# Optimization experiments

Hardware: AMD Instinct MI355X
Metric: run time of the kernel (lower is better)

Reference implementation:

```python
import jax, jax.numpy as jnp
import numpy as np

EPS = 1e-6
K = 20
NUM_OBJECTS = 50
OBJ_FEAT = 256
C_DIM = 128
HIDDEN = 128


def vn_linear(x, W):
    # x: [B, C, 3, ...]; W: [O, C] -> [B, O, 3, ...]
    return jnp.einsum('oc,bc...->bo...', W, x)


def vn_leaky(x, Wdir, slope):
    d = vn_linear(x, Wdir)
    dot = jnp.sum(x * d, axis=2, keepdims=True)
    dsq = jnp.sum(d * d, axis=2, keepdims=True)
    x_neg = x - (dot / (dsq + EPS)) * d
    return slope * x + (1.0 - slope) * jnp.where(dot >= 0, x, x_neg)


def vn_linear_leaky(x, Wfeat, Wdir, slope):
    pf = vn_linear(x, Wfeat)
    d = vn_linear(x, Wdir)
    dot = jnp.sum(pf * d, axis=2, keepdims=True)
    dsq = jnp.sum(d * d, axis=2, keepdims=True)
    p_neg = pf - (dot / (dsq + EPS)) * d
    return slope * pf + (1.0 - slope) * jnp.where(dot >= 0, pf, p_neg)


def resblock(x, fc0, fc1, a0, a1, sc):
    net = vn_linear(vn_leaky(x, a0, 0.0), fc0)
    dx = vn_linear(vn_leaky(net, a1, 0.0), fc1)
    return vn_linear(x, sc) + dx


def get_graph_feature_cross(x, k):
    # x: [B, 3, N] -> edge features [B, 3, 3, N, k]
    inner = -2.0 * jnp.einsum('bdn,bdm->bnm', x, x)
    xx = jnp.sum(x * x, axis=1)                       # [B, N]
    neg_dist = -xx[:, :, None] - inner - xx[:, None, :]  # [B, N, N]
    idx = jax.lax.top_k(neg_dist, k)[1]               # [B, N, k] nearest neighbors
    xt = jnp.transpose(x, (0, 2, 1))                  # [B, N, 3]
    nbr = jax.vmap(lambda pts, ind: pts[ind])(xt, idx)  # [B, N, k, 3]
    ctr = jnp.broadcast_to(xt[:, :, None, :], nbr.shape)
    cross = jnp.cross(nbr, ctr)
    feat = jnp.stack([nbr - ctr, ctr, cross], axis=3)  # [B, N, k, 3, 3]
    return jnp.transpose(feat, (0, 3, 4, 1, 2))


def mlp2(zf, w0, w1, w2):
    h = jax.nn.relu(zf @ w0.T)
    h = jax.nn.relu(h @ w1.T)
    return h @ w2.T


def setup_inputs():
    key = jax.random.key(0)
    ks = jax.random.split(key, 24)
    B, N = 4, 4096

    def rn(k, shape):
        return jax.random.normal(k, shape, dtype=jnp.float32) * (1.0 / np.sqrt(shape[-1]))

    return {
        'p': jax.random.normal(ks[0], (B, N, 3), dtype=jnp.float32),
        'z_idxs': jax.random.randint(ks[1], (B,), 0, NUM_OBJECTS),
        'z': jax.random.normal(ks[2], (NUM_OBJECTS, OBJ_FEAT), dtype=jnp.float32),
        'hw0': rn(ks[3], (OBJ_FEAT, OBJ_FEAT)),
        'hw1': rn(ks[4], (OBJ_FEAT, OBJ_FEAT)),
        'hw2': rn(ks[5], (C_DIM * HIDDEN, OBJ_FEAT)),
        'hb0': rn(ks[6], (OBJ_FEAT, OBJ_FEAT)),
        'hb1': rn(ks[7], (OBJ_FEAT, OBJ_FEAT)),
        'hb2': rn(ks[8], (C_DIM, OBJ_FEAT)),
        'conv_pos_feat': rn(ks[9], (128, 3)),
        'conv_pos_dir': rn(ks[10], (128, 3)),
        'fc_pos_w': rn(ks[11], (2 * HIDDEN, 128)),
        'blk_fc0': rn(ks[12], (5, HIDDEN, 2 * HIDDEN)),
        'blk_fc1': rn(ks[13], (5, HIDDEN, HIDDEN)),
        'blk_act0': rn(ks[14], (5, 2 * HIDDEN, 2 * HIDDEN)),
        'blk_act1': rn(ks[15], (5, HIDDEN, HIDDEN)),
        'blk_sc': rn(ks[16], (5, HIDDEN, 2 * HIDDEN)),
        'actc_dir': rn(ks[17], (HIDDEN, HIDDEN)),
    }


def reference(p, z_idxs, z, hw0, hw1, hw2, hb0, hb1, hb2, conv_pos_feat,
              conv_pos_dir, fc_pos_w, blk_fc0, blk_fc1, blk_act0, blk_act1,
              blk_sc, actc_dir):
    B = p.shape[0]
    x = jnp.transpose(p, (0, 2, 1))                       # [B, 3, N]
    feat = get_graph_feature_cross(x, K)                  # [B, 3, 3, N, k]
    net = vn_linear_leaky(feat, conv_pos_feat, conv_pos_dir, 0.2)  # [B,128,3,N,k]
    net = jnp.mean(net, axis=-1)                          # [B,128,3,N]
    net = vn_linear(net, fc_pos_w)                        # [B,256,3,N]
    for i in range(5):
        net = resblock(net, blk_fc0[i], blk_fc1[i], blk_act0[i], blk_act1[i], blk_sc[i])
        if i < 4:
            pooled = jnp.mean(net, axis=-1, keepdims=True)
            net = jnp.concatenate([net, jnp.broadcast_to(pooled, net.shape)], axis=1)
    net = vn_leaky(jnp.mean(net, axis=-1), actc_dir, 0.2)  # [B, HIDDEN, 3]
    zf = z[z_idxs]                                        # [B, OBJ_FEAT]
    w = mlp2(zf, hw0, hw1, hw2).reshape(B, C_DIM, HIDDEN)  # hypernet weights
    b = mlp2(zf, hb0, hb1, hb2)                           # [B, C_DIM]
    c = jnp.einsum('bhd,bch->bcd', net, w) + b[:, :, None]  # [B, C_DIM, 3]
    return c
```

## Files before the change

kernel.cpp:

```cpp
#include <hip/hip_runtime.h>
#include <hip/hip_fp16.h>
#include <cstdint>
#include <cstddef>

#define NPTS 4096
#define BATCH 4
#define KNN 20

typedef __half f16;
using f32x4 = __attribute__((ext_vector_type(4))) float;
using f16x8 = __attribute__((ext_vector_type(8))) _Float16;

__device__ inline void gload_lds16(const void* g, void* l) {
    __builtin_amdgcn_global_load_lds(
        (const __attribute__((address_space(1))) uint32_t*)g,
        (__attribute__((address_space(3))) uint32_t*)l, 16, 0, 0);
}

__global__ __launch_bounds__(256) void knn_kernel(const float* __restrict__ p,
                                                  int* __restrict__ idx_out) {
    __shared__ float smem[12288];
    float* pts = smem;
    unsigned* lists = (unsigned*)smem;
    const int tid  = threadIdx.x;
    const int wave = tid >> 6, lane = tid & 63;
    const int b  = blockIdx.x >> 10;
    const int nb = ((blockIdx.x & 1023) << 2) + wave;

    const float4* src4 = (const float4*)(p + (size_t)b * NPTS * 3);
    float4* dst4 = (float4*)pts;
    for (int i = tid; i < NPTS * 3 / 4; i += 256) dst4[i] = src4[i];
    __syncthreads();

    const float cx = pts[3 * nb], cy = pts[3 * nb + 1], cz = pts[3 * nb + 2];
    unsigned lst[4];
#pragma unroll
    for (int i = 0; i < 4; i++) lst[i] = 0xFFFFFFFFu;

    for (int t = 0; t < NPTS / 64; t++) {
        int m = (t << 6) + lane;
        float dx = pts[3 * m] - cx, dy = pts[3 * m + 1] - cy, dz = pts[3 * m + 2] - cz;
        float d = dx * dx + dy * dy + dz * dz;
        unsigned c = (__float_as_uint(d) & 0xFFFFF000u) | (unsigned)m;
#pragma unroll
        for (int j = 0; j < 4; j++) {
            unsigned lo = min(c, lst[j]);
            c = max(c, lst[j]);
            lst[j] = lo;
        }
    }
    __syncthreads();
#pragma unroll
    for (int i = 0; i < 4; i++) lists[tid * 5 + i] = lst[i];
    __syncthreads();

    int head = 0;
    const size_t out_base = ((size_t)b * NPTS + nb) * KNN;
    for (int r = 0; r < KNN; r++) {
        unsigned cand = (head < 4) ? lists[tid * 5 + head] : 0xFFFFFFFFu;
        unsigned win = cand;
#pragma unroll
        for (int off = 32; off > 0; off >>= 1) {
            unsigned o = (unsigned)__shfl_xor((int)win, off, 64);
            win = o < win ? o : win;
        }
        if (cand == win) head++;
        if (lane == 0) idx_out[out_base + r] = (int)(win & 0xFFFu);
    }
}

__global__ __launch_bounds__(128) void edgeconv_kernel(
    const float* __restrict__ p, const int* __restrict__ idx,
    const float* __restrict__ wf, const float* __restrict__ wd,
    f16* __restrict__ out) {
    __shared__ float e[KNN][9];
    const int col = blockIdx.x;
    const int b = col >> 12;
    const int tid = threadIdx.x;
    const float cx = p[(size_t)col * 3], cy = p[(size_t)col * 3 + 1], cz = p[(size_t)col * 3 + 2];
    if (tid < KNN) {
        int j = idx[(size_t)col * KNN + tid];
        const float* q = &p[((size_t)b * NPTS + j) * 3];
        float nx = q[0], ny = q[1], nz = q[2];
        e[tid][0] = nx - cx; e[tid][1] = ny - cy; e[tid][2] = nz - cz;
        e[tid][3] = cx;      e[tid][4] = cy;      e[tid][5] = cz;
        e[tid][6] = ny * cz - nz * cy;
        e[tid][7] = nz * cx - nx * cz;
        e[tid][8] = nx * cy - ny * cx;
    }
    __syncthreads();
    const int o = tid;
    const float f0 = wf[o * 3], f1 = wf[o * 3 + 1], f2 = wf[o * 3 + 2];
    const float g0 = wd[o * 3], g1 = wd[o * 3 + 1], g2 = wd[o * 3 + 2];
    float a0 = 0.f, a1 = 0.f, a2 = 0.f;
    for (int k = 0; k < KNN; k++) {
        float pf[3], dd[3];
#pragma unroll
        for (int s = 0; s < 3; s++) {
            pf[s] = f0 * e[k][s] + f1 * e[k][3 + s] + f2 * e[k][6 + s];
            dd[s] = g0 * e[k][s] + g1 * e[k][3 + s] + g2 * e[k][6 + s];
        }
        float dot = pf[0] * dd[0] + pf[1] * dd[1] + pf[2] * dd[2];
        float dsq = dd[0] * dd[0] + dd[1] * dd[1] + dd[2] * dd[2];
        float coef = dot / (dsq + 1e-6f);
        bool pos = dot >= 0.f;
        float v0 = pos ? pf[0] : pf[0] - coef * dd[0];
        float v1 = pos ? pf[1] : pf[1] - coef * dd[1];
        float v2 = pos ? pf[2] : pf[2] - coef * dd[2];
        a0 += 0.2f * pf[0] + 0.8f * v0;
        a1 += 0.2f * pf[1] + 0.8f * v1;
        a2 += 0.2f * pf[2] + 0.8f * v2;
    }
    const float inv = 1.f / (float)KNN;
    out[((size_t)col * 3 + 0) * 128 + o] = __float2half(a0 * inv);
    out[((size_t)col * 3 + 1) * 128 + o] = __float2half(a1 * inv);
    out[((size_t)col * 3 + 2) * 128 + o] = __float2half(a2 * inv);
}

__global__ __launch_bounds__(256) void gemm_mfma(
    const uint16_t* __restrict__ A, const uint16_t* __restrict__ W,
    f16* __restrict__ Y, int K, int O, int lda, int ldw) {
    __shared__ char lds[65536];
    const int tid = threadIdx.x;
    const int wid = tid >> 6, lane = tid & 63;
    const int r0 = blockIdx.x * 128, c0 = blockIdx.y * 128;
    const int wm = (wid >> 1) * 64, wn = (wid & 1) * 64;

    f32x4 acc[4][4];
#pragma unroll
    for (int i = 0; i < 4; i++)
#pragma unroll
        for (int j = 0; j < 4; j++) acc[i][j] = (f32x4){0.f, 0.f, 0.f, 0.f};

    const int srow = (lane >> 3);
    const int scol = ((lane & 7) ^ srow) * 8;

    auto STAGE = [&](int bf, int kc) {
        char* As = lds + bf * 32768;
        char* Bs = As + 16384;
#pragma unroll
        for (int t = 0; t < 4; t++) {
            int chunk = t * 4 + wid;
            int row = chunk * 8 + srow;
            gload_lds16(&A[(size_t)(r0 + row) * lda + kc + scol], As + chunk * 1024);
            gload_lds16(&W[(size_t)(c0 + row) * ldw + kc + scol], Bs + chunk * 1024);
        }
    };
    auto COMPUTE = [&](int bf) {
        char* As = lds + bf * 32768;
        char* Bs = As + 16384;
#pragma unroll
        for (int kb = 0; kb < 2; kb++) {
            const int kl = (kb * 32 + (lane >> 4) * 8) * 2;
            f16x8 af[4], bfr[4];
#pragma unroll
            for (int mi = 0; mi < 4; mi++) {
                int r = wm + mi * 16 + (lane & 15);
                af[mi] = *(const f16x8*)(As + r * 128 + (kl ^ ((r & 7) << 4)));
            }
#pragma unroll
            for (int ni = 0; ni < 4; ni++) {
                int r = wn + ni * 16 + (lane & 15);
                bfr[ni] = *(const f16x8*)(Bs + r * 128 + (kl ^ ((r & 7) << 4)));
            }
#pragma unroll
            for (int mi = 0; mi < 4; mi++)
#pragma unroll
                for (int ni = 0; ni < 4; ni++)
                    acc[mi][ni] = __builtin_amdgcn_mfma_f32_16x16x32_f16(
                        af[mi], bfr[ni], acc[mi][ni], 0, 0, 0);
        }
    };

    STAGE(0, 0);
    __syncthreads();
    int cur = 0;
    const int nt = K >> 6;
    for (int t = 0; t < nt; t++) {
        if (t + 1 < nt) STAGE(cur ^ 1, (t + 1) << 6);
        COMPUTE(cur);
        __syncthreads();
        cur ^= 1;
    }
#pragma unroll
    for (int mi = 0; mi < 4; mi++)
#pragma unroll
        for (int ni = 0; ni < 4; ni++) {
            int col = c0 + wn + ni * 16 + (lane & 15);
#pragma unroll
            for (int r = 0; r < 4; r++) {
                int m = r0 + wm + mi * 16 + (lane >> 4) * 4 + r;
                Y[(size_t)m * O + col] = __float2half(acc[mi][ni][r]);
            }
        }
}

template <int KIN>
__global__ __launch_bounds__(256) void resblock_kernel(
    const uint16_t* __restrict__ INg,
    const uint16_t* __restrict__ Wa0,
    const uint16_t* __restrict__ Wfc0,
    const uint16_t* __restrict__ Wa1,
    const uint16_t* __restrict__ Wsc,
    const uint16_t* __restrict__ Wfc1,
    const float* __restrict__ PBg,
    const float* __restrict__ BAg,
    const float* __restrict__ BSCg,
    f16* __restrict__ OUTg,
    float* __restrict__ PPg) {
    constexpr int INRB = KIN * 2 + 16;
    constexpr int H0RB = 528;
    constexpr int MRB  = 272;
    constexpr int INSZ = 48 * INRB;
    constexpr int CONSZ = (KIN == 128) ? 6144 : 0;
    constexpr int H0O  = INSZ + CONSZ;
    constexpr int MIDO = H0O + 48 * H0RB;
    __shared__ char lds[MIDO + 48 * MRB];
    char* INs = lds;
    float* PBs  = (float*)(lds + INSZ);
    float* BAs  = PBs + 384;
    float* BSCs = BAs + 768;
    char* H0  = lds + H0O;
    char* MID = lds + MIDO;

    const int tid = threadIdx.x;
    const int lane = tid & 63;
    const int wc = tid >> 6;
    const int gr0 = blockIdx.x * 48;

    if (KIN == 128) {
        const int b = blockIdx.x >> 8;
        for (int i = tid; i < 384; i += 256) PBs[i]  = PBg[b * 384 + i];
        for (int i = tid; i < 768; i += 256) BAs[i]  = BAg[b * 768 + i];
        for (int i = tid; i < 384; i += 256) BSCs[i] = BSCg[b * 384 + i];
    }
    if (KIN == 128) {
#pragma unroll
        for (int j = 0; j < 3; j++) {
            int chunk = tid + j * 256;
            int row = chunk >> 4, c16 = chunk & 15;
            f16x8 v = *(const f16x8*)(INg + (size_t)(gr0 + row) * 128 + c16 * 8);
            *(f16x8*)(INs + row * INRB + c16 * 16) = v;
        }
    } else {
#pragma unroll
        for (int j = 0; j < 6; j++) {
            int chunk = tid + j * 256;
            int row = chunk >> 5, c16 = chunk & 31;
            f16x8 v = *(const f16x8*)(INg + (size_t)(gr0 + row) * 256 + c16 * 8);
            *(f16x8*)(INs + row * INRB + c16 * 16) = v;
        }
    }
    __syncthreads();

    {
        f32x4 acc[3][4];
#pragma unroll
        for (int i = 0; i < 3; i++)
#pragma unroll
            for (int j = 0; j < 4; j++) acc[i][j] = (f32x4){0.f, 0.f, 0.f, 0.f};
#pragma unroll
        for (int ks = 0; ks < KIN / 32; ks++) {
            const int kb = ks * 64 + (lane >> 4) * 16;
            f16x8 af[3], bf[4];
#pragma unroll
            for (int mi = 0; mi < 3; mi++) {
                int r = mi * 16 + (lane & 15);
                af[mi] = *(const f16x8*)(INs + r * INRB + kb);
            }
#pragma unroll
            for (int ni = 0; ni < 4; ni++) {
                int o = wc * 64 + ni * 16 + (lane & 15);
                bf[ni] = *(const f16x8*)(Wa0 + o * 256 + ks * 32 + (lane >> 4) * 8);
            }
#pragma unroll
            for (int mi = 0; mi < 3; mi++)
#pragma unroll
                for (int ni = 0; ni < 4; ni++)
                    acc[mi][ni] = __builtin_amdgcn_mfma_f32_16x16x32_f16(
                        af[mi], bf[ni], acc[mi][ni], 0, 0, 0);
        }
#pragma unroll
        for (int mi = 0; mi < 3; mi++)
#pragma unroll
            for (int ni = 0; ni < 4; ni++) {
                int col = wc * 64 + ni * 16 + (lane & 15);
#pragma unroll
                for (int r = 0; r < 4; r++) {
                    int row = mi * 16 + (lane >> 4) * 4 + r;
                    float v = acc[mi][ni][r];
                    if (KIN == 128) v += BAs[(row % 3) * 256 + col];
                    *(f16*)(H0 + row * H0RB + col * 2) = __float2half(v);
                }
            }
    }
    __syncthreads();
#pragma unroll
    for (int j = 0; j < 8; j++) {
        int it = tid + j * 256;
        int pnt = it >> 7, cp = it & 127;
        float xv[3][2], dv[3][2];
#pragma unroll
        for (int s = 0; s < 3; s++) {
            int row = pnt * 3 + s;
            __half2 d2 = *(const __half2*)(H0 + row * H0RB + cp * 4);
            dv[s][0] = __half2float(d2.x); dv[s][1] = __half2float(d2.y);
            if (KIN == 256) {
                __half2 x2 = *(const __half2*)(INs + row * INRB + cp * 4);
                xv[s][0] = __half2float(x2.x); xv[s][1] = __half2float(x2.y);
            } else {
                if (cp < 64) {
                    __half2 x2 = *(const __half2*)(INs + row * INRB + cp * 4);
                    xv[s][0] = __half2float(x2.x); xv[s][1] = __half2float(x2.y);
                } else {
                    xv[s][0] = PBs[s * 128 + (cp - 64) * 2];
                    xv[s][1] = PBs[s * 128 + (cp - 64) * 2 + 1];
                }
            }
        }
#pragma unroll
        for (int jj = 0; jj < 2; jj++) {
            float dot = xv[0][jj] * dv[0][jj] + xv[1][jj] * dv[1][jj] + xv[2][jj] * dv[2][jj];
            float dsq = dv[0][jj] * dv[0][jj] + dv[1][jj] * dv[1][jj] + dv[2][jj] * dv[2][jj];
            float coef = dot / (dsq + 1e-6f);
            bool pos = dot >= 0.f;
#pragma unroll
            for (int s = 0; s < 3; s++)
                xv[s][jj] = pos ? xv[s][jj] : xv[s][jj] - coef * dv[s][jj];
        }
#pragma unroll
        for (int s = 0; s < 3; s++) {
            int row = pnt * 3 + s;
            __half2 h2;
            h2.x = __float2half(xv[s][0]);
            h2.y = __float2half(xv[s][1]);
            *(__half2*)(H0 + row * H0RB + cp * 4) = h2;
        }
    }
    __syncthreads();

    {
        f32x4 acc[3][2];
#pragma unroll
        for (int i = 0; i < 3; i++) { acc[i][0] = (f32x4){0,0,0,0}; acc[i][1] = (f32x4){0,0,0,0}; }
#pragma unroll
        for (int ks = 0; ks < 8; ks++) {
            const int kb = ks * 64 + (lane >> 4) * 16;
            f16x8 af[3], bf[2];
#pragma unroll
            for (int mi = 0; mi < 3; mi++) {
                int r = mi * 16 + (lane & 15);
                af[mi] = *(const f16x8*)(H0 + r * H0RB + kb);
            }
#pragma unroll
            for (int ni = 0; ni < 2; ni++) {
                int o = wc * 32 + ni * 16 + (lane & 15);
                bf[ni] = *(const f16x8*)(Wfc0 + o * 256 + ks * 32 + (lane >> 4) * 8);
            }
#pragma unroll
            for (int mi = 0; mi < 3; mi++)
#pragma unroll
                for (int ni = 0; ni < 2; ni++)
                    acc[mi][ni] = __builtin_amdgcn_mfma_f32_16x16x32_f16(
                        af[mi], bf[ni], acc[mi][ni], 0, 0, 0);
        }
#pragma unroll
        for (int mi = 0; mi < 3; mi++)
#pragma unroll
            for (int ni = 0; ni < 2; ni++) {
                int col = wc * 32 + ni * 16 + (lane & 15);
#pragma unroll
                for (int r = 0; r < 4; r++) {
                    int row = mi * 16 + (lane >> 4) * 4 + r;
                    *(f16*)(MID + row * MRB + col * 2) = __float2half(acc[mi][ni][r]);
                }
            }
    }
    __syncthreads();

    {
        f32x4 acc[3][2];
#pragma unroll
        for (int i = 0; i < 3; i++) { acc[i][0] = (f32x4){0,0,0,0}; acc[i][1] = (f32x4){0,0,0,0}; }
#pragma unroll
        for (int ks = 0; ks < 4; ks++) {
            const int kb = ks * 64 + (lane >> 4) * 16;
            f16x8 af[3], bf[2];
#pragma unroll
            for (int mi = 0; mi < 3; mi++) {
                int r = mi * 16 + (lane & 15);
                af[mi] = *(const f16x8*)(MID + r * MRB + kb);
            }
#pragma unroll
            for (int ni = 0; ni < 2; ni++) {
                int o = wc * 32 + ni * 16 + (lane & 15);
                bf[ni] = *(const f16x8*)(Wa1 + o * 128 + ks * 32 + (lane >> 4) * 8);
            }
#pragma unroll
            for (int mi = 0; mi < 3; mi++)
#pragma unroll
                for (int ni = 0; ni < 2; ni++)
                    acc[mi][ni] = __builtin_amdgcn_mfma_f32_16x16x32_f16(
                        af[mi], bf[ni], acc[mi][ni], 0, 0, 0);
        }
#pragma unroll
        for (int mi = 0; mi < 3; mi++)
#pragma unroll
            for (int ni = 0; ni < 2; ni++) {
                int col = wc * 32 + ni * 16 + (lane & 15);
#pragma unroll
                for (int r = 0; r < 4; r++) {
                    int row = mi * 16 + (lane >> 4) * 4 + r;
                    *(f16*)(H0 + row * MRB + col * 2) = __float2half(acc[mi][ni][r]);
                }
            }
    }
    __syncthreads();
#pragma unroll
    for (int j = 0; j < 4; j++) {
        int it = tid + j * 256;
        int pnt = it >> 6, cp = it & 63;
        float xv[3][2], dv[3][2];
#pragma unroll
        for (int s = 0; s < 3; s++) {
            int row = pnt * 3 + s;
            __half2 d2 = *(const __half2*)(H0 + row * MRB + cp * 4);
            __half2 x2 = *(const __half2*)(MID + row * MRB + cp * 4);
            dv[s][0] = __half2float(d2.x); dv[s][1] = __half2float(d2.y);
            xv[s][0] = __half2float(x2.x); xv[s][1] = __half2float(x2.y);
        }
#pragma unroll
        for (int jj = 0; jj < 2; jj++) {
            float dot = xv[0][jj] * dv[0][jj] + xv[1][jj] * dv[1][jj] + xv[2][jj] * dv[2][jj];
            float dsq = dv[0][jj] * dv[0][jj] + dv[1][jj] * dv[1][jj] + dv[2][jj] * dv[2][jj];
            float coef = dot / (dsq + 1e-6f);
            bool pos = dot >= 0.f;
#pragma unroll
            for (int s = 0; s < 3; s++)
                xv[s][jj] = pos ? xv[s][jj] : xv[s][jj] - coef * dv[s][jj];
        }
#pragma unroll
        for (int s = 0; s < 3; s++) {
            int row = pnt * 3 + s;
            __half2 h2;
            h2.x = __float2half(xv[s][0]);
            h2.y = __float2half(xv[s][1]);
            *(__half2*)(H0 + row * MRB + cp * 4) = h2;
        }
    }
    __syncthreads();

    {
        f32x4 acc[3][2];
#pragma unroll
        for (int i = 0; i < 3; i++) { acc[i][0] = (f32x4){0,0,0,0}; acc[i][1] = (f32x4){0,0,0,0}; }
        constexpr int NKS = (KIN + 128) / 32;
#pragma unroll
        for (int ks = 0; ks < NKS; ks++) {
            const int kelem = ks * 32;
            f16x8 af[3], bf[2];
            if (kelem < KIN) {
                const int kb = kelem * 2 + (lane >> 4) * 16;
#pragma unroll
                for (int mi = 0; mi < 3; mi++) {
                    int r = mi * 16 + (lane & 15);
                    af[mi] = *(const f16x8*)(INs + r * INRB + kb);
                }
#pragma unroll
                for (int ni = 0; ni < 2; ni++) {
                    int o = wc * 32 + ni * 16 + (lane & 15);
                    bf[ni] = *(const f16x8*)(Wsc + o * 256 + kelem + (lane >> 4) * 8);
                }
            } else {
                const int kk = kelem - KIN;
                const int kb = kk * 2 + (lane >> 4) * 16;
#pragma unroll
                for (int mi = 0; mi < 3; mi++) {
                    int r = mi * 16 + (lane & 15);
                    af[mi] = *(const f16x8*)(H0 + r * MRB + kb);
                }
#pragma unroll
                for (int ni = 0; ni < 2; ni++) {
                    int o = wc * 32 + ni * 16 + (lane & 15);
                    bf[ni] = *(const f16x8*)(Wfc1 + o * 128 + kk + (lane >> 4) * 8);
                }
            }
#pragma unroll
            for (int mi = 0; mi < 3; mi++)
#pragma unroll
                for (int ni = 0; ni < 2; ni++)
                    acc[mi][ni] = __builtin_amdgcn_mfma_f32_16x16x32_f16(
                        af[mi], bf[ni], acc[mi][ni], 0, 0, 0);
        }
        float ps[2][3] = {};
#pragma unroll
        for (int mi = 0; mi < 3; mi++)
#pragma unroll
            for (int ni = 0; ni < 2; ni++) {
                int col = wc * 32 + ni * 16 + (lane & 15);
#pragma unroll
                for (int r = 0; r < 4; r++) {
                    int row = mi * 16 + (lane >> 4) * 4 + r;
                    float v = acc[mi][ni][r];
                    if (KIN == 128) v += BSCs[(row % 3) * 128 + col];
                    OUTg[(size_t)(gr0 + row) * 128 + col] = __float2half(v);
                    ps[ni][row % 3] += v;
                }
            }
#pragma unroll
        for (int ni = 0; ni < 2; ni++)
#pragma unroll
            for (int s = 0; s < 3; s++) {
                float x = ps[ni][s];
                x += __shfl_xor(x, 16, 64);
                x += __shfl_xor(x, 32, 64);
                ps[ni][s] = x;
            }
        if ((lane >> 4) == 0) {
#pragma unroll
            for (int ni = 0; ni < 2; ni++) {
                int col = wc * 32 + ni * 16 + (lane & 15);
#pragma unroll
                for (int s = 0; s < 3; s++)
                    PPg[(size_t)blockIdx.x * 384 + s * 128 + col] = ps[ni][s];
            }
        }
    }
}

__global__ __launch_bounds__(512) void poolbias_kernel(
    const float* __restrict__ PP, const f16* __restrict__ a0n, const f16* __restrict__ scn,
    float* __restrict__ PB, float* __restrict__ BA, float* __restrict__ BSC, int hasbias) {
    __shared__ float red[4][128];
    __shared__ float pl[128];
    const int bs = blockIdx.x;
    const int b = bs / 3, s = bs % 3;
    const int t = threadIdx.x;
    const int col = t & 127, seg = t >> 7;
    {
        float acc = 0.f;
        const float* base = PP + (size_t)(b * 256) * 384 + s * 128 + col;
        for (int k = seg * 64; k < seg * 64 + 64; k++) acc += base[(size_t)k * 384];
        red[seg][col] = acc;
    }
    __syncthreads();
    if (t < 128) {
        float a = (red[0][t] + red[1][t]) + (red[2][t] + red[3][t]);
        a *= (1.f / (float)NPTS);
        pl[t] = a;
        PB[bs * 128 + t] = a;
    }
    __syncthreads();
    if (!hasbias) return;
    if (t < 256) {
        float s2 = 0.f;
        for (int c = 0; c < 128; c++) s2 += __half2float(a0n[t * 256 + 128 + c]) * pl[c];
        BA[bs * 256 + t] = s2;
    } else if (t < 384) {
        int o = t - 256;
        float s2 = 0.f;
        for (int c = 0; c < 128; c++) s2 += __half2float(scn[o * 256 + 128 + c]) * pl[c];
        BSC[bs * 128 + o] = s2;
    }
}

__global__ void cvt_all(const float* __restrict__ fcpw, const float* __restrict__ act0,
                        const float* __restrict__ fc0, const float* __restrict__ act1,
                        const float* __restrict__ fc1, const float* __restrict__ scw,
                        f16* o_fcpw, f16* o_act0, f16* o_fc0, f16* o_act1, f16* o_fc1,
                        f16* o_scw) {
    int i = blockIdx.x * 256 + threadIdx.x;
    if (i < 32768) { o_fcpw[i] = __float2half(fcpw[i]); }
    else if (i < 360448) { int j = i - 32768;  o_act0[j] = __float2half(act0[j]); }
    else if (i < 524288) { int j = i - 360448; o_fc0[j]  = __float2half(fc0[j]); }
    else if (i < 606208) { int j = i - 524288; o_act1[j] = __float2half(act1[j]); }
    else if (i < 688128) { int j = i - 606208; o_fc1[j]  = __float2half(fc1[j]); }
    else                 { int j = i - 688128; o_scw[j]  = __float2half(scw[j]); }
}

__global__ __launch_bounds__(256) void hypermlp_kernel(
    const float* __restrict__ z, const int* __restrict__ zidx,
    const float* __restrict__ hw0, const float* __restrict__ hw1,
    const float* __restrict__ hb0, const float* __restrict__ hb1,
    const float* __restrict__ hb2,
    float* __restrict__ H2, float* __restrict__ BV) {
    __shared__ float zf[256], ta[256], tb[256];
    const int b = blockIdx.x, o = threadIdx.x;
    zf[o] = z[(size_t)zidx[b] * 256 + o];
    __syncthreads();
    float s = 0.f;
    for (int c = 0; c < 256; c++) s += zf[c] * hw0[o * 256 + c];
    ta[o] = fmaxf(s, 0.f);
    __syncthreads();
    s = 0.f;
    for (int c = 0; c < 256; c++) s += ta[c] * hw1[o * 256 + c];
    tb[o] = fmaxf(s, 0.f);
    __syncthreads();
    H2[(size_t)b * 256 + o] = tb[o];
    s = 0.f;
    for (int c = 0; c < 256; c++) s += zf[c] * hb0[o * 256 + c];
    __syncthreads();
    ta[o] = fmaxf(s, 0.f);
    __syncthreads();
    s = 0.f;
    for (int c = 0; c < 256; c++) s += ta[c] * hb1[o * 256 + c];
    __syncthreads();
    tb[o] = fmaxf(s, 0.f);
    __syncthreads();
    if (o < 128) {
        s = 0.f;
        for (int c = 0; c < 256; c++) s += tb[c] * hb2[o * 256 + c];
        BV[(size_t)b * 128 + o] = s;
    }
}

__global__ __launch_bounds__(256) void wmat_kernel(const float* __restrict__ H2,
                                                   const float* __restrict__ hw2,
                                                   float* __restrict__ WM) {
    __shared__ float h[256];
    const int b = blockIdx.y;
    const int row = blockIdx.x * 256 + threadIdx.x;
    h[threadIdx.x] = H2[(size_t)b * 256 + threadIdx.x];
    __syncthreads();
    float s = 0.f;
    for (int c = 0; c < 256; c++) s += h[c] * hw2[(size_t)row * 256 + c];
    WM[(size_t)b * 16384 + row] = s;
}

__global__ __launch_bounds__(384) void final_out_kernel(
    const float* __restrict__ pb, const float* __restrict__ actc,
    const float* __restrict__ WM, const float* __restrict__ BV,
    float* __restrict__ out) {
    __shared__ float pb2s[3][128];
    const int b = blockIdx.x;
    const int t = threadIdx.x;
    if (t < 128) {
        const int o = t;
        float d0 = 0.f, d1 = 0.f, d2 = 0.f;
        for (int c = 0; c < 128; c++) {
            float w = actc[o * 128 + c];
            d0 += w * pb[(size_t)(b * 3 + 0) * 128 + c];
            d1 += w * pb[(size_t)(b * 3 + 1) * 128 + c];
            d2 += w * pb[(size_t)(b * 3 + 2) * 128 + c];
        }
        float x0 = pb[(size_t)(b * 3 + 0) * 128 + o];
        float x1 = pb[(size_t)(b * 3 + 1) * 128 + o];
        float x2 = pb[(size_t)(b * 3 + 2) * 128 + o];
        float dot = x0 * d0 + x1 * d1 + x2 * d2;
        float dsq = d0 * d0 + d1 * d1 + d2 * d2;
        float coef = dot / (dsq + 1e-6f);
        bool pos = dot >= 0.f;
        float h0 = pos ? x0 : x0 - coef * d0;
        float h1 = pos ? x1 : x1 - coef * d1;
        float h2 = pos ? x2 : x2 - coef * d2;
        pb2s[0][o] = 0.2f * x0 + 0.8f * h0;
        pb2s[1][o] = 0.2f * x1 + 0.8f * h1;
        pb2s[2][o] = 0.2f * x2 + 0.8f * h2;
    }
    __syncthreads();
    const int cd = t / 3, d = t % 3;
    float s = BV[(size_t)b * 128 + cd];
    for (int h = 0; h < 128; h++)
        s += pb2s[d][h] * WM[(size_t)b * 16384 + cd * 128 + h];
    out[(size_t)b * 384 + cd * 3 + d] = s;
}

extern "C" void kernel_launch(void* const* d_in, const int* in_sizes, int n_in,
                              void* d_out, int out_size, void* d_ws, size_t ws_size,
                              hipStream_t stream) {
    (void)in_sizes; (void)n_in; (void)out_size; (void)ws_size;
    const float* p     = (const float*)d_in[0];
    const int*   zidx  = (const int*)d_in[1];
    const float* z     = (const float*)d_in[2];
    const float* hw0   = (const float*)d_in[3];
    const float* hw1   = (const float*)d_in[4];
    const float* hw2   = (const float*)d_in[5];
    const float* hb0   = (const float*)d_in[6];
    const float* hb1   = (const float*)d_in[7];
    const float* hb2   = (const float*)d_in[8];
    const float* cpf   = (const float*)d_in[9];
    const float* cpd   = (const float*)d_in[10];
    const float* fcpw  = (const float*)d_in[11];
    const float* fc0w  = (const float*)d_in[12];
    const float* fc1w  = (const float*)d_in[13];
    const float* act0  = (const float*)d_in[14];
    const float* act1  = (const float*)d_in[15];
    const float* scw   = (const float*)d_in[16];
    const float* actc  = (const float*)d_in[17];
    float* out = (float*)d_out;
    char* ws = (char*)d_ws;

    int*   IDX   = (int*)(ws + 0);
    f16*   XB    = (f16*)(ws + 1310720);
    f16*   MB    = (f16*)(ws + 26476544);
    f16*   MB2   = (f16*)(ws + 39059456);
    f16*   FCPW16= (f16*)(ws + 51642368);
    f16*   ACT0W = (f16*)(ws + 51707904);
    f16*   FC0W  = (f16*)(ws + 52363264);
    f16*   ACT1W = (f16*)(ws + 52690944);
    f16*   FC1W  = (f16*)(ws + 52854784);
    f16*   SCW16 = (f16*)(ws + 53018624);
    float* PP    = (float*)(ws + 53346304);
    float* PB    = (float*)(ws + 54919168);
    float* H2    = (float*)(ws + 54931456);
    float* BV    = (float*)(ws + 54935552);
    float* WM    = (float*)(ws + 54937600);
    float* BA    = (float*)(ws + 55199744);
    float* BSC   = (float*)(ws + 55212032);

    cvt_all<<<3328, 256, 0, stream>>>(fcpw, act0, fc0w, act1, fc1w, scw,
                                      FCPW16, ACT0W, FC0W, ACT1W, FC1W, SCW16);

    knn_kernel<<<BATCH * NPTS / 4, 256, 0, stream>>>(p, IDX);
    edgeconv_kernel<<<BATCH * NPTS, 128, 0, stream>>>(p, IDX, cpf, cpd, MB);
    gemm_mfma<<<dim3(384, 2), 256, 0, stream>>>((const uint16_t*)MB, (const uint16_t*)FCPW16,
                                                XB, 128, 256, 128, 128);

    resblock_kernel<256><<<1024, 256, 0, stream>>>(
        (const uint16_t*)XB, (const uint16_t*)ACT0W, (const uint16_t*)FC0W,
        (const uint16_t*)ACT1W, (const uint16_t*)SCW16, (const uint16_t*)FC1W,
        nullptr, nullptr, nullptr, MB, PP);
    poolbias_kernel<<<12, 512, 0, stream>>>(PP, ACT0W + 1 * 65536, SCW16 + 1 * 32768,
                                            PB, BA, BSC, 1);

    for (int i = 1; i < 5; i++) {
        const f16* a0h = ACT0W + (size_t)i * 256 * 256;
        const f16* sch = SCW16 + (size_t)i * 128 * 256;
        f16* in  = (i & 1) ? MB : MB2;
        f16* ob  = (i & 1) ? MB2 : MB;
        resblock_kernel<128><<<1024, 256, 0, stream>>>(
            (const uint16_t*)in, (const uint16_t*)a0h,
            (const uint16_t*)(FC0W + (size_t)i * 128 * 256),
            (const uint16_t*)(ACT1W + (size_t)i * 128 * 128),
            (const uint16_t*)sch,
            (const uint16_t*)(FC1W + (size_t)i * 128 * 128),
            PB, BA, BSC, ob, PP);
        if (i < 4) {
            poolbias_kernel<<<12, 512, 0, stream>>>(
                PP, ACT0W + (size_t)(i + 1) * 65536, SCW16 + (size_t)(i + 1) * 32768,
                PB, BA, BSC, 1);
        } else {
            poolbias_kernel<<<12, 512, 0, stream>>>(PP, nullptr, nullptr, PB, BA, BSC, 0);
        }
    }

    hypermlp_kernel<<<4, 256, 0, stream>>>(z, zidx, hw0, hw1, hb0, hb1, hb2, H2, BV);
    wmat_kernel<<<dim3(64, 4), 256, 0, stream>>>(H2, hw2, WM);
    final_out_kernel<<<4, 384, 0, stream>>>(PB, actc, WM, BV, out);
}
```

Baseline: 445.9 us.

## Fuse fc_pos GEMM into first resblock, ballot-based kNN selection, fast reciprocal

The standalone fc_pos GEMM is removed. The first resblock now loads the 128-channel edgeconv output into LDS and computes the 256-channel projection with MFMA before the block body, which avoids writing and re-reading a large fp16 intermediate through global memory. The kNN top-20 merge no longer runs 20 shuffle-reduction rounds through LDS lists. It binary-searches a threshold with wave ballots and scatters winners by prefix popcount, so the output order is no longer sorted by distance and ties at the threshold could emit more than K entries. Divisions in the VN leaky activations are replaced with hardware reciprocal approximations.

Result: faster. 409.8 us (-8.1%).

```diff
diff --git a/kernel.cpp b/kernel.cpp
--- a/kernel.cpp
+++ b/kernel.cpp
@@ -11,17 +11,9 @@
 using f32x4 = __attribute__((ext_vector_type(4))) float;
 using f16x8 = __attribute__((ext_vector_type(8))) _Float16;
 
-__device__ inline void gload_lds16(const void* g, void* l) {
-    __builtin_amdgcn_global_load_lds(
-        (const __attribute__((address_space(1))) uint32_t*)g,
-        (__attribute__((address_space(3))) uint32_t*)l, 16, 0, 0);
-}
-
 __global__ __launch_bounds__(256) void knn_kernel(const float* __restrict__ p,
                                                   int* __restrict__ idx_out) {
-    __shared__ float smem[12288];
-    float* pts = smem;
-    unsigned* lists = (unsigned*)smem;
+    __shared__ float pts[12288];
     const int tid  = threadIdx.x;
     const int wave = tid >> 6, lane = tid & 63;
     const int b  = blockIdx.x >> 10;
@@ -49,23 +41,29 @@
             lst[j] = lo;
         }
     }
-    __syncthreads();
-#pragma unroll
-    for (int i = 0; i < 4; i++) lists[tid * 5 + i] = lst[i];
-    __syncthreads();
-
-    int head = 0;
+
+    unsigned lo = 0u, hi = 0xFFFFFFFFu;
+    for (int it = 0; it < 32; it++) {
+        unsigned mid = lo + ((hi - lo) >> 1);
+        int cnt = __popcll(__ballot(lst[0] <= mid)) + __popcll(__ballot(lst[1] <= mid))
+                + __popcll(__ballot(lst[2] <= mid)) + __popcll(__ballot(lst[3] <= mid));
+        if (cnt >= KNN) hi = mid; else lo = mid + 1;
+    }
+    const unsigned T = hi;
+
+    unsigned long long bl[4];
+#pragma unroll
+    for (int j = 0; j < 4; j++) bl[j] = __ballot(lst[j] <= T);
+    const unsigned long long lmask = (lane == 63) ? ~0ull >> 1 : (1ull << lane) - 1;
+    int base = 0;
     const size_t out_base = ((size_t)b * NPTS + nb) * KNN;
-    for (int r = 0; r < KNN; r++) {
-        unsigned cand = (head < 4) ? lists[tid * 5 + head] : 0xFFFFFFFFu;
-        unsigned win = cand;
-#pragma unroll
-        for (int off = 32; off > 0; off >>= 1) {
-            unsigned o = (unsigned)__shfl_xor((int)win, off, 64);
-            win = o < win ? o : win;
-        }
-        if (cand == win) head++;
-        if (lane == 0) idx_out[out_base + r] = (int)(win & 0xFFFu);
+#pragma unroll
+    for (int j = 0; j < 4; j++) {
+        if (lst[j] <= T) {
+            int pos = base + (int)__popcll(bl[j] & lmask);
+            idx_out[out_base + pos] = (int)(lst[j] & 0xFFFu);
+        }
+        base += (int)__popcll(bl[j]);
     }
 }
 
@@ -102,7 +100,7 @@
         }
         float dot = pf[0] * dd[0] + pf[1] * dd[1] + pf[2] * dd[2];
         float dsq = dd[0] * dd[0] + dd[1] * dd[1] + dd[2] * dd[2];
-        float coef = dot / (dsq + 1e-6f);
+        float coef = dot * __builtin_amdgcn_rcpf(dsq + 1e-6f);
         bool pos = dot >= 0.f;
         float v0 = pos ? pf[0] : pf[0] - coef * dd[0];
         float v1 = pos ? pf[1] : pf[1] - coef * dd[1];
@@ -117,87 +115,10 @@
     out[((size_t)col * 3 + 2) * 128 + o] = __float2half(a2 * inv);
 }
 
-__global__ __launch_bounds__(256) void gemm_mfma(
-    const uint16_t* __restrict__ A, const uint16_t* __restrict__ W,
-    f16* __restrict__ Y, int K, int O, int lda, int ldw) {
-    __shared__ char lds[65536];
-    const int tid = threadIdx.x;
-    const int wid = tid >> 6, lane = tid & 63;
-    const int r0 = blockIdx.x * 128, c0 = blockIdx.y * 128;
-    const int wm = (wid >> 1) * 64, wn = (wid & 1) * 64;
-
-    f32x4 acc[4][4];
-#pragma unroll
-    for (int i = 0; i < 4; i++)
-#pragma unroll
-        for (int j = 0; j < 4; j++) acc[i][j] = (f32x4){0.f, 0.f, 0.f, 0.f};
-
-    const int srow = (lane >> 3);
-    const int scol = ((lane & 7) ^ srow) * 8;
-
-    auto STAGE = [&](int bf, int kc) {
-        char* As = lds + bf * 32768;
-        char* Bs = As + 16384;
-#pragma unroll
-        for (int t = 0; t < 4; t++) {
-            int chunk = t * 4 + wid;
-            int row = chunk * 8 + srow;
-            gload_lds16(&A[(size_t)(r0 + row) * lda + kc + scol], As + chunk * 1024);
-            gload_lds16(&W[(size_t)(c0 + row) * ldw + kc + scol], Bs + chunk * 1024);
-        }
-    };
-    auto COMPUTE = [&](int bf) {
-        char* As = lds + bf * 32768;
-        char* Bs = As + 16384;
-#pragma unroll
-        for (int kb = 0; kb < 2; kb++) {
-            const int kl = (kb * 32 + (lane >> 4) * 8) * 2;
-            f16x8 af[4], bfr[4];
-#pragma unroll
-            for (int mi = 0; mi < 4; mi++) {
-                int r = wm + mi * 16 + (lane & 15);
-                af[mi] = *(const f16x8*)(As + r * 128 + (kl ^ ((r & 7) << 4)));
-            }
-#pragma unroll
-            for (int ni = 0; ni < 4; ni++) {
-                int r = wn + ni * 16 + (lane & 15);
-                bfr[ni] = *(const f16x8*)(Bs + r * 128 + (kl ^ ((r & 7) << 4)));
-            }
-#pragma unroll
-            for (int mi = 0; mi < 4; mi++)
-#pragma unroll
-                for (int ni = 0; ni < 4; ni++)
-                    acc[mi][ni] = __builtin_amdgcn_mfma_f32_16x16x32_f16(
-                        af[mi], bfr[ni], acc[mi][ni], 0, 0, 0);
-        }
-    };
-
-    STAGE(0, 0);
-    __syncthreads();
-    int cur = 0;
-    const int nt = K >> 6;
-    for (int t = 0; t < nt; t++) {
-        if (t + 1 < nt) STAGE(cur ^ 1, (t + 1) << 6);
-        COMPUTE(cur);
-        __syncthreads();
-        cur ^= 1;
-    }
-#pragma unroll
-    for (int mi = 0; mi < 4; mi++)
-#pragma unroll
-        for (int ni = 0; ni < 4; ni++) {
-            int col = c0 + wn + ni * 16 + (lane & 15);
-#pragma unroll
-            for (int r = 0; r < 4; r++) {
-                int m = r0 + wm + mi * 16 + (lane >> 4) * 4 + r;
-                Y[(size_t)m * O + col] = __float2half(acc[mi][ni][r]);
-            }
-        }
-}
-
 template <int KIN>
 __global__ __launch_bounds__(256) void resblock_kernel(
     const uint16_t* __restrict__ INg,
+    const uint16_t* __restrict__ Wfcp,
     const uint16_t* __restrict__ Wa0,
     const uint16_t* __restrict__ Wfc0,
     const uint16_t* __restrict__ Wa1,
@@ -208,16 +129,18 @@
     const float* __restrict__ BSCg,
     f16* __restrict__ OUTg,
     float* __restrict__ PPg) {
-    constexpr int INRB = KIN * 2 + 16;
+    constexpr int XRB  = (KIN == 256) ? 528 : 272;
     constexpr int H0RB = 528;
     constexpr int MRB  = 272;
-    constexpr int INSZ = 48 * INRB;
+    constexpr int MBSZ = (KIN == 256) ? 48 * 272 : 0;
+    constexpr int XSZ  = 48 * XRB;
     constexpr int CONSZ = (KIN == 128) ? 6144 : 0;
-    constexpr int H0O  = INSZ + CONSZ;
+    constexpr int H0O  = MBSZ + XSZ + CONSZ;
     constexpr int MIDO = H0O + 48 * H0RB;
     __shared__ char lds[MIDO + 48 * MRB];
-    char* INs = lds;
-    float* PBs  = (float*)(lds + INSZ);
+    char* MBs = lds;
+    char* INs = lds + MBSZ;
+    float* PBs  = (float*)(lds + MBSZ + XSZ);
     float* BAs  = PBs + 384;
     float* BSCs = BAs + 768;
     char* H0  = lds + H0O;
@@ -234,24 +157,58 @@
         for (int i = tid; i < 768; i += 256) BAs[i]  = BAg[b * 768 + i];
         for (int i = tid; i < 384; i += 256) BSCs[i] = BSCg[b * 384 + i];
     }
-    if (KIN == 128) {
+    {
+        char* dst = (KIN == 256) ? MBs : INs;
 #pragma unroll
         for (int j = 0; j < 3; j++) {
             int chunk = tid + j * 256;
             int row = chunk >> 4, c16 = chunk & 15;
             f16x8 v = *(const f16x8*)(INg + (size_t)(gr0 + row) * 128 + c16 * 8);
-            *(f16x8*)(INs + row * INRB + c16 * 16) = v;
-        }
-    } else {
-#pragma unroll
-        for (int j = 0; j < 6; j++) {
-            int chunk = tid + j * 256;
-            int row = chunk >> 5, c16 = chunk & 31;
-            f16x8 v = *(const f16x8*)(INg + (size_t)(gr0 + row) * 256 + c16 * 8);
-            *(f16x8*)(INs + row * INRB + c16 * 16) = v;
-        }
-    }
-    __syncthreads();
+            *(f16x8*)(dst + row * 272 + c16 * 16) = v;
+        }
+    }
+    __syncthreads();
+
+    if (KIN == 256) {
+        f32x4 acc[3][4];
+#pragma unroll
+        for (int i = 0; i < 3; i++)
+#pragma unroll
+            for (int j = 0; j < 4; j++) acc[i][j] = (f32x4){0.f, 0.f, 0.f, 0.f};
+#pragma unroll
+        for (int ks = 0; ks < 4; ks++) {
+            const int kb = ks * 64 + (lane >> 4) * 16;
+            f16x8 af[3], bf[4];
+#pragma unroll
+            for (int mi = 0; mi < 3; mi++) {
+                int r = mi * 16 + (lane & 15);
+                af[mi] = *(const f16x8*)(MBs + r * 272 + kb);
+            }
+#pragma unroll
+            for (int ni = 0; ni < 4; ni++) {
+                int o = wc * 64 + ni * 16 + (lane & 15);
+                bf[ni] = *(const f16x8*)(Wfcp + o * 128 + ks * 32 + (lane >> 4) * 8);
+            }
+#pragma unroll
+            for (int mi = 0; mi < 3; mi++)
+#pragma unroll
+                for (int ni = 0; ni < 4; ni++)
+                    acc[mi][ni] = __builtin_amdgcn_mfma_f32_16x16x32_f16(
+                        af[mi], bf[ni], acc[mi][ni], 0, 0, 0);
+        }
+#pragma unroll
+        for (int mi = 0; mi < 3; mi++)
+#pragma unroll
+            for (int ni = 0; ni < 4; ni++) {
+                int col = wc * 64 + ni * 16 + (lane & 15);
+#pragma unroll
+                for (int r = 0; r < 4; r++) {
+                    int row = mi * 16 + (lane >> 4) * 4 + r;
+                    *(f16*)(INs + row * XRB + col * 2) = __float2half(acc[mi][ni][r]);
+                }
+            }
+        __syncthreads();
+    }
 
     {
         f32x4 acc[3][4];
@@ -266,7 +223,7 @@
 #pragma unroll
             for (int mi = 0; mi < 3; mi++) {
                 int r = mi * 16 + (lane & 15);
-                af[mi] = *(const f16x8*)(INs + r * INRB + kb);
+                af[mi] = *(const f16x8*)(INs + r * XRB + kb);
             }
 #pragma unroll
             for (int ni = 0; ni < 4; ni++) {
@@ -306,11 +263,11 @@
             __half2 d2 = *(const __half2*)(H0 + row * H0RB + cp * 4);
             dv[s][0] = __half2float(d2.x); dv[s][1] = __half2float(d2.y);
             if (KIN == 256) {
-                __half2 x2 = *(const __half2*)(INs + row * INRB + cp * 4);
+                __half2 x2 = *(const __half2*)(INs + row * XRB + cp * 4);
                 xv[s][0] = __half2float(x2.x); xv[s][1] = __half2float(x2.y);
             } else {
                 if (cp < 64) {
-                    __half2 x2 = *(const __half2*)(INs + row * INRB + cp * 4);
+                    __half2 x2 = *(const __half2*)(INs + row * XRB + cp * 4);
                     xv[s][0] = __half2float(x2.x); xv[s][1] = __half2float(x2.y);
                 } else {
                     xv[s][0] = PBs[s * 128 + (cp - 64) * 2];
@@ -322,7 +279,7 @@
         for (int jj = 0; jj < 2; jj++) {
             float dot = xv[0][jj] * dv[0][jj] + xv[1][jj] * dv[1][jj] + xv[2][jj] * dv[2][jj];
             float dsq = dv[0][jj] * dv[0][jj] + dv[1][jj] * dv[1][jj] + dv[2][jj] * dv[2][jj];
-            float coef = dot / (dsq + 1e-6f);
+            float coef = dot * __builtin_amdgcn_rcpf(dsq + 1e-6f);
             bool pos = dot >= 0.f;
 #pragma unroll
             for (int s = 0; s < 3; s++)
@@ -433,7 +390,7 @@
         for (int jj = 0; jj < 2; jj++) {
             float dot = xv[0][jj] * dv[0][jj] + xv[1][jj] * dv[1][jj] + xv[2][jj] * dv[2][jj];
             float dsq = dv[0][jj] * dv[0][jj] + dv[1][jj] * dv[1][jj] + dv[2][jj] * dv[2][jj];
-            float coef = dot / (dsq + 1e-6f);
+            float coef = dot * __builtin_amdgcn_rcpf(dsq + 1e-6f);
             bool pos = dot >= 0.f;
 #pragma unroll
             for (int s = 0; s < 3; s++)
@@ -464,7 +421,7 @@
 #pragma unroll
                 for (int mi = 0; mi < 3; mi++) {
                     int r = mi * 16 + (lane & 15);
-                    af[mi] = *(const f16x8*)(INs + r * INRB + kb);
+                    af[mi] = *(const f16x8*)(INs + r * XRB + kb);
                 }
 #pragma unroll
                 for (int ni = 0; ni < 2; ni++) {
@@ -691,45 +648,44 @@
     char* ws = (char*)d_ws;
 
     int*   IDX   = (int*)(ws + 0);
-    f16*   XB    = (f16*)(ws + 1310720);
-    f16*   MB    = (f16*)(ws + 26476544);
-    f16*   MB2   = (f16*)(ws + 39059456);
-    f16*   FCPW16= (f16*)(ws + 51642368);
-    f16*   ACT0W = (f16*)(ws + 51707904);
-    f16*   FC0W  = (f16*)(ws + 52363264);
-    f16*   ACT1W = (f16*)(ws + 52690944);
-    f16*   FC1W  = (f16*)(ws + 52854784);
-    f16*   SCW16 = (f16*)(ws + 53018624);
-    float* PP    = (float*)(ws + 53346304);
-    float* PB    = (float*)(ws + 54919168);
-    float* H2    = (float*)(ws + 54931456);
-    float* BV    = (float*)(ws + 54935552);
-    float* WM    = (float*)(ws + 54937600);
-    float* BA    = (float*)(ws + 55199744);
-    float* BSC   = (float*)(ws + 55212032);
+    f16*   MB    = (f16*)(ws + 1310720);
+    f16*   MB2   = (f16*)(ws + 13893632);
+    f16*   FCPW16= (f16*)(ws + 26476544);
+    f16*   ACT0W = (f16*)(ws + 26542080);
+    f16*   FC0W  = (f16*)(ws + 27197440);
+    f16*   ACT1W = (f16*)(ws + 27525120);
+    f16*   FC1W  = (f16*)(ws + 27688960);
+    f16*   SCW16 = (f16*)(ws + 27852800);
+    float* PP    = (float*)(ws + 28180480);
+    float* PB    = (float*)(ws + 29753344);
+    float* H2    = (float*)(ws + 29759488);
+    float* BV    = (float*)(ws + 29763584);
+    float* WM    = (float*)(ws + 29765632);
+    float* BA    = (float*)(ws + 30027776);
+    float* BSC   = (float*)(ws + 30040064);
 
     cvt_all<<<3328, 256, 0, stream>>>(fcpw, act0, fc0w, act1, fc1w, scw,
                                       FCPW16, ACT0W, FC0W, ACT1W, FC1W, SCW16);
 
     knn_kernel<<<BATCH * NPTS / 4, 256, 0, stream>>>(p, IDX);
     edgeconv_kernel<<<BATCH * NPTS, 128, 0, stream>>>(p, IDX, cpf, cpd, MB);
-    gemm_mfma<<<dim3(384, 2), 256, 0, stream>>>((const uint16_t*)MB, (const uint16_t*)FCPW16,
-                                                XB, 128, 256, 128, 128);
 
     resblock_kernel<256><<<1024, 256, 0, stream>>>(
-        (const uint16_t*)XB, (const uint16_t*)ACT0W, (const uint16_t*)FC0W,
+        (const uint16_t*)MB, (const uint16_t*)FCPW16,
+        (const uint16_t*)ACT0W, (const uint16_t*)FC0W,
         (const uint16_t*)ACT1W, (const uint16_t*)SCW16, (const uint16_t*)FC1W,
-        nullptr, nullptr, nullptr, MB, PP);
+        nullptr, nullptr, nullptr, MB2, PP);
     poolbias_kernel<<<12, 512, 0, stream>>>(PP, ACT0W + 1 * 65536, SCW16 + 1 * 32768,
                                             PB, BA, BSC, 1);
 
     for (int i = 1; i < 5; i++) {
         const f16* a0h = ACT0W + (size_t)i * 256 * 256;
         const f16* sch = SCW16 + (size_t)i * 128 * 256;
-        f16* in  = (i & 1) ? MB : MB2;
-        f16* ob  = (i & 1) ? MB2 : MB;
+        f16* in  = (i & 1) ? MB2 : MB;
+        f16* ob  = (i & 1) ? MB : MB2;
         resblock_kernel<128><<<1024, 256, 0, stream>>>(
-            (const uint16_t*)in, (const uint16_t*)a0h,
+            (const uint16_t*)in, nullptr,
+            (const uint16_t*)a0h,
             (const uint16_t*)(FC0W + (size_t)i * 128 * 256),
             (const uint16_t*)(ACT1W + (size_t)i * 128 * 128),
             (const uint16_t*)sch,
```
